# Performance work log

Measured on AMD Instinct MI355X. Metric: run time of the kernel, lower is better.

## Reference

```python
import jax, jax.numpy as jnp
import numpy as np

D = 2048          # hidden_size
N = 16            # num query heads
K = 8             # num kv heads
G = N // K        # GQA groups
H = 128           # head_dim (== head_dim_original, already padded)
T_NOISE = 1024
T_PAD = 1024
MAX_KV = 4096
THETA = 1000000.0
EPS = 1e-6
SM_SCALE = H ** -0.5
NEG = -1e30


def apply_rope(x, pos):
    # x: (T, heads, H); rotate-half (NeoX/Qwen) convention over full head_dim
    half = H // 2
    inv_freq = 1.0 / (THETA ** (jnp.arange(half, dtype=jnp.float32) / half))
    ang = pos.astype(jnp.float32)[:, None] * inv_freq[None, :]      # (T, half)
    cos = jnp.cos(ang)[:, None, :]
    sin = jnp.sin(ang)[:, None, :]
    x1, x2 = x[..., :half], x[..., half:]
    return jnp.concatenate([x1 * cos - x2 * sin, x2 * cos + x1 * sin], axis=-1)


def rms_norm(x, scale):
    var = jnp.mean(jnp.square(x), axis=-1, keepdims=True)
    return x * jax.lax.rsqrt(var + EPS) * scale


def setup_inputs() -> dict:
    key = jax.random.key(0)
    ks = jax.random.split(key, 10)
    cache_len = 1024
    actual_ctx = 768
    u = lambda k, shape: jax.random.uniform(k, shape, jnp.float32) * 0.01  # nnx uniform init
    return {
        "x_noise": jax.random.normal(ks[0], (T_NOISE, D), jnp.float32),
        "target_hidden": jax.random.normal(ks[1], (T_PAD, D), jnp.float32),
        "noise_positions": jnp.arange(T_NOISE, dtype=jnp.int32) + cache_len + actual_ctx,
        "ctx_positions": jnp.arange(T_PAD, dtype=jnp.int32) + cache_len,
        "kv_cache_k": jax.random.normal(ks[2], (1, N, MAX_KV, H), jnp.float32),
        "kv_cache_v": jax.random.normal(ks[3], (1, N, MAX_KV, H), jnp.float32),
        "cache_len": cache_len,
        "actual_ctx_count": actual_ctx,
        "Wq": u(ks[4], (D, N, H)),
        "Wk": u(ks[5], (D, K, H)),
        "Wv": u(ks[6], (D, K, H)),
        "Wo": u(ks[7], (N, H, D)),
        "q_scale": u(ks[8], (H,)),
        "k_scale": u(ks[9], (H,)),
    }


def reference(x_noise, target_hidden, noise_positions, ctx_positions,
              kv_cache_k, kv_cache_v, cache_len, actual_ctx_count,
              Wq, Wk, Wv, Wo, q_scale, k_scale):
    T_noise = x_noise.shape[0]
    T_padded = target_hidden.shape[0]
    # Q projection + RMSNorm + RoPE
    q = jnp.einsum('td,dnh->tnh', x_noise, Wq)
    q = apply_rope(rms_norm(q, q_scale), noise_positions)              # (Tq, N, H)
    # K/V over [context, noise]
    x_new = jnp.concatenate([target_hidden, x_noise], axis=0)
    k_new = jnp.einsum('td,dkh->tkh', x_new, Wk)
    v_new = jnp.einsum('td,dkh->tkh', x_new, Wv)
    new_positions = jnp.concatenate([ctx_positions, noise_positions], axis=0)
    k_new = apply_rope(rms_norm(k_new, k_scale), new_positions)
    # GQA expand before cache write (matches original)
    if G > 1:
        k_new = jnp.repeat(k_new, G, axis=1)
        v_new = jnp.repeat(v_new, G, axis=1)
    # Phase A: masked context write at cache_len
    ctx_mask = (jnp.arange(T_padded) < actual_ctx_count)[:, None, None]
    k_ctx = jnp.where(ctx_mask, k_new[:T_padded], 0.0)
    v_ctx = jnp.where(ctx_mask, v_new[:T_padded], 0.0)
    to4d = lambda a: a.transpose(1, 0, 2)[None]                        # (1, N, T, H)
    kv_cache_k = jax.lax.dynamic_update_slice(kv_cache_k, to4d(k_ctx), (0, 0, cache_len, 0))
    kv_cache_v = jax.lax.dynamic_update_slice(kv_cache_v, to4d(v_ctx), (0, 0, cache_len, 0))
    # Phase B: noise write at cache_len + actual_ctx_count
    noise_start = cache_len + actual_ctx_count
    kv_cache_k = jax.lax.dynamic_update_slice(kv_cache_k, to4d(k_new[T_padded:]), (0, 0, noise_start, 0))
    kv_cache_v = jax.lax.dynamic_update_slice(kv_cache_v, to4d(v_new[T_padded:]), (0, 0, noise_start, 0))
    new_cache_len = noise_start + T_noise
    # Non-causal attention over full cache, padding masked (segment_ids semantics)
    kv_valid = jnp.arange(MAX_KV) < new_cache_len                      # (MAX_KV,)
    scores = jnp.einsum('qnh,nkh->nqk', q, kv_cache_k[0]) * SM_SCALE   # (N, Tq, MAX_KV)
    scores = jnp.where(kv_valid[None, None, :], scores, NEG)
    probs = jax.nn.softmax(scores, axis=-1)
    attn = jnp.einsum('nqk,nkh->qnh', probs, kv_cache_v[0])            # (Tq, N, H)
    output = jnp.einsum('qnh,nhd->qd', attn, Wo)                       # (Tq, D)
    return (output, kv_cache_k, kv_cache_v)
```

## Files before the change

### kernel.cpp

```cpp
#include <hip/hip_runtime.h>
#include <hip/hip_bf16.h>
#include <math.h>

#define D 2048
#define NH 16
#define KHD 8
#define HD 128
#define T_NOISE 1024
#define T_PAD 1024
#define MAX_KV 4096
#define SM_SCALE 0.08838834764831845f

typedef __attribute__((ext_vector_type(8))) short short8;
typedef __attribute__((ext_vector_type(4))) short short4v;
typedef __attribute__((ext_vector_type(4))) float f32x4;

__device__ __forceinline__ unsigned short f2bf(float f) {
    union { float f; unsigned u; } v; v.f = f;
    unsigned r = v.u + 0x7fff + ((v.u >> 16) & 1);
    return (unsigned short)(r >> 16);
}
__device__ __forceinline__ float bf2f(short s) {
    union { unsigned u; float f; } v; v.u = ((unsigned)(unsigned short)s) << 16;
    return v.f;
}
__device__ __forceinline__ void gload16(const void* g, void* l) {
    __builtin_amdgcn_global_load_lds(
        (const __attribute__((address_space(1))) unsigned int*)g,
        (__attribute__((address_space(3))) unsigned int*)l, 16, 0, 0);
}
__device__ __forceinline__ unsigned cvtpk(float lo, float hi) {
    unsigned r;
    asm("v_cvt_pk_bf16_f32 %0, %1, %2" : "=v"(r) : "v"(lo), "v"(hi));
    return r;
}

__global__ __launch_bounds__(256)
void cast_concat(const float* __restrict__ A0, const float* __restrict__ A1,
                 short* __restrict__ out, int splitElems) {
    int i = (blockIdx.x * 256 + threadIdx.x) * 8;
    const float* src = (i < splitElems) ? (A0 + i) : (A1 + (i - splitElems));
    float4 f0 = *(const float4*)src;
    float4 f1 = *(const float4*)(src + 4);
    short8 s;
    s[0] = (short)f2bf(f0.x); s[1] = (short)f2bf(f0.y);
    s[2] = (short)f2bf(f0.z); s[3] = (short)f2bf(f0.w);
    s[4] = (short)f2bf(f1.x); s[5] = (short)f2bf(f1.y);
    s[6] = (short)f2bf(f1.z); s[7] = (short)f2bf(f1.w);
    *(short8*)(out + i) = s;
}

__global__ __launch_bounds__(256)
void conv_transpose(const float* __restrict__ W, short* __restrict__ Wt,
                    int R, int C) {
    __shared__ short t[64][72];
    int tid = threadIdx.x;
    int r0 = blockIdx.y * 64, c0 = blockIdx.x * 64;
    int rl = tid >> 4, cl4 = (tid & 15) * 4;
    #pragma unroll
    for (int j = 0; j < 4; ++j) {
        int r = rl + j * 16;
        float4 f = *(const float4*)(W + (size_t)(r0 + r) * C + c0 + cl4);
        t[cl4 + 0][r] = (short)f2bf(f.x);
        t[cl4 + 1][r] = (short)f2bf(f.y);
        t[cl4 + 2][r] = (short)f2bf(f.z);
        t[cl4 + 3][r] = (short)f2bf(f.w);
    }
    __syncthreads();
    #pragma unroll
    for (int j = 0; j < 2; ++j) {
        int idx = tid + j * 256;
        int cr = idx >> 3, rc8 = (idx & 7) * 8;
        *(short8*)(Wt + (size_t)(c0 + cr) * R + r0 + rc8) = *(const short8*)&t[cr][rc8];
    }
}

__global__ __launch_bounds__(256)
void gemm_qkv(const short* __restrict__ xbf, const short* __restrict__ Btp,
              short* __restrict__ k_tmpb, short* __restrict__ v_tmpb,
              short* __restrict__ q_tmpb) {
    const int n0 = blockIdx.x * 128;
    const int m0 = blockIdx.y * 128;
    const bool isQ = (n0 >= 2048);
    if (isQ && m0 >= 1024) return;
    const short* A = xbf + (isQ ? (size_t)1024 * 2048 : 0);

    __shared__ __align__(16) short As[128 * 32];
    __shared__ __align__(16) short Bs[128 * 32];
    const int tid = threadIdx.x;
    const int w = tid >> 6, lane = tid & 63;
    const int g = lane >> 4, li = lane & 15;
    const int wr = w >> 1, wc = w & 1;

    f32x4 acc[4][4];
    #pragma unroll
    for (int mi = 0; mi < 4; ++mi)
        #pragma unroll
        for (int ni = 0; ni < 4; ++ni) {
            acc[mi][ni][0] = 0.f; acc[mi][ni][1] = 0.f;
            acc[mi][ni][2] = 0.f; acc[mi][ni][3] = 0.f;
        }

    for (int k0 = 0; k0 < 2048; k0 += 32) {
        #pragma unroll
        for (int i = 0; i < 2; ++i) {
            int idx = i * 256 + w * 64 + lane;
            int row = idx >> 2, slot = idx & 3;
            gload16(A + (size_t)(m0 + row) * 2048 + k0 + slot * 8,
                    (char*)As + (size_t)(i * 256 + w * 64) * 16);
            gload16(Btp + (size_t)(n0 + row) * 2048 + k0 + slot * 8,
                    (char*)Bs + (size_t)(i * 256 + w * 64) * 16);
        }
        __syncthreads();
        short8 af[4], bf[4];
        #pragma unroll
        for (int mi = 0; mi < 4; ++mi)
            af[mi] = *(const short8*)&As[(wr * 64 + mi * 16 + li) * 32 + g * 8];
        #pragma unroll
        for (int ni = 0; ni < 4; ++ni)
            bf[ni] = *(const short8*)&Bs[(wc * 64 + ni * 16 + li) * 32 + g * 8];
        #pragma unroll
        for (int mi = 0; mi < 4; ++mi)
            #pragma unroll
            for (int ni = 0; ni < 4; ++ni)
                acc[mi][ni] = __builtin_amdgcn_mfma_f32_16x16x32_bf16(
                    af[mi], bf[ni], acc[mi][ni], 0, 0, 0);
        __syncthreads();
    }
    short* cp; int cbase, ldc2;
    if (n0 < 1024)      { cp = k_tmpb; cbase = 0;    ldc2 = 1024; }
    else if (n0 < 2048) { cp = v_tmpb; cbase = 1024; ldc2 = 1024; }
    else                { cp = q_tmpb; cbase = 2048; ldc2 = 2048; }
    #pragma unroll
    for (int mi = 0; mi < 4; ++mi)
        #pragma unroll
        for (int ni = 0; ni < 4; ++ni) {
            int n = n0 + wc * 64 + ni * 16 + li - cbase;
            #pragma unroll
            for (int r = 0; r < 4; ++r) {
                int m = m0 + wr * 64 + mi * 16 + 4 * g + r;
                cp[(size_t)m * ldc2 + n] = (short)f2bf(acc[mi][ni][r]);
            }
        }
}

__global__ __launch_bounds__(256)
void gemm_bf16(const short* __restrict__ A, const short* __restrict__ Bt,
               float* __restrict__ C0, float* __restrict__ C1,
               int csplit, int ldc, int K, int M) {
    __shared__ __align__(16) short As[128 * 32];
    __shared__ __align__(16) short Bs[128 * 32];
    const int tid = threadIdx.x;
    const int w = tid >> 6, lane = tid & 63;
    const int g = lane >> 4, li = lane & 15;
    const int wr = w >> 1, wc = w & 1;
    const int m0 = blockIdx.y * 128, n0 = blockIdx.x * 128;

    f32x4 acc[4][4];
    #pragma unroll
    for (int mi = 0; mi < 4; ++mi)
        #pragma unroll
        for (int ni = 0; ni < 4; ++ni) {
            acc[mi][ni][0] = 0.f; acc[mi][ni][1] = 0.f;
            acc[mi][ni][2] = 0.f; acc[mi][ni][3] = 0.f;
        }

    for (int k0 = 0; k0 < K; k0 += 32) {
        #pragma unroll
        for (int i = 0; i < 2; ++i) {
            int idx = i * 256 + w * 64 + lane;
            int row = idx >> 2, slot = idx & 3;
            gload16(A + (size_t)(m0 + row) * K + k0 + slot * 8,
                    (char*)As + (size_t)(i * 256 + w * 64) * 16);
            gload16(Bt + (size_t)(n0 + row) * K + k0 + slot * 8,
                    (char*)Bs + (size_t)(i * 256 + w * 64) * 16);
        }
        __syncthreads();
        short8 af[4], bf[4];
        #pragma unroll
        for (int mi = 0; mi < 4; ++mi)
            af[mi] = *(const short8*)&As[(wr * 64 + mi * 16 + li) * 32 + g * 8];
        #pragma unroll
        for (int ni = 0; ni < 4; ++ni)
            bf[ni] = *(const short8*)&Bs[(wc * 64 + ni * 16 + li) * 32 + g * 8];
        #pragma unroll
        for (int mi = 0; mi < 4; ++mi)
            #pragma unroll
            for (int ni = 0; ni < 4; ++ni)
                acc[mi][ni] = __builtin_amdgcn_mfma_f32_16x16x32_bf16(
                    af[mi], bf[ni], acc[mi][ni], 0, 0, 0);
        __syncthreads();
    }
    #pragma unroll
    for (int mi = 0; mi < 4; ++mi) {
        #pragma unroll
        for (int ni = 0; ni < 4; ++ni) {
            int n = n0 + wc * 64 + ni * 16 + li;
            float* cp; int cn;
            if (n < csplit) { cp = C0; cn = n; } else { cp = C1; cn = n - csplit; }
            #pragma unroll
            for (int r = 0; r < 4; ++r) {
                int m = m0 + wr * 64 + mi * 16 + 4 * g + r;
                cp[(size_t)m * ldc + cn] = acc[mi][ni][r];
            }
        }
    }
}

__global__ __launch_bounds__(128)
void rmsrope_bf(short* __restrict__ x, int hpt,
                const int* __restrict__ posA, const int* __restrict__ posB,
                int splitT, const float* __restrict__ scale, float post) {
    __shared__ float red[128];
    __shared__ float nrm[128];
    int row = blockIdx.x;
    int h = threadIdx.x;
    float v = bf2f(x[(size_t)row * HD + h]);
    red[h] = v * v;
    __syncthreads();
    #pragma unroll
    for (int off = 64; off > 0; off >>= 1) {
        if (h < off) red[h] += red[h + off];
        __syncthreads();
    }
    float inv = rsqrtf(red[0] * (1.0f / 128.0f) + 1e-6f);
    nrm[h] = v * inv * scale[h];
    __syncthreads();
    if (h < 64) {
        int t = row / hpt;
        int pos = (t < splitT) ? posA[t] : posB[t - splitT];
        float inv_freq = expf((float)h * (-13.815510557964274f / 64.0f));
        float ang = (float)pos * inv_freq;
        float c = cosf(ang), s = sinf(ang);
        float x1 = nrm[h], x2 = nrm[h + 64];
        x[(size_t)row * HD + h]      = (short)f2bf((x1 * c - x2 * s) * post);
        x[(size_t)row * HD + h + 64] = (short)f2bf((x2 * c + x1 * s) * post);
    }
}

__global__ __launch_bounds__(256)
void cache_scatter2(const float* __restrict__ in_k, const float* __restrict__ in_v,
                    const short* __restrict__ k_tmpb, const short* __restrict__ v_tmpb,
                    float* __restrict__ out_k, float* __restrict__ out_v,
                    short* __restrict__ kbf, short* __restrict__ vbf,
                    const int* __restrict__ clp, const int* __restrict__ acp) {
    const int cache_len = clp[0], actx = acp[0];
    const int noise_start = cache_len + actx;
    const int new_len = noise_start + T_NOISE;
    int i = blockIdx.x * 256 + threadIdx.x;
    int n = i >> 16;
    int rem = i & 65535;
    int pos = rem >> 4;
    int h8 = (rem & 15) << 3;
    size_t co = ((size_t)(n * MAX_KV + pos)) * HD + h8;
    short8 ks8, vs8;
    if (pos >= cache_len && pos < new_len) {
        int tkn = (pos < noise_start) ? (pos - cache_len) : (T_PAD + (pos - noise_start));
        size_t so = ((size_t)(tkn * KHD + (n >> 1))) * HD + h8;
        ks8 = *(const short8*)(k_tmpb + so);
        vs8 = *(const short8*)(v_tmpb + so);
        float4 a, b;
        a.x = bf2f(ks8[0]); a.y = bf2f(ks8[1]); a.z = bf2f(ks8[2]); a.w = bf2f(ks8[3]);
        b.x = bf2f(ks8[4]); b.y = bf2f(ks8[5]); b.z = bf2f(ks8[6]); b.w = bf2f(ks8[7]);
        *(float4*)(out_k + co) = a; *(float4*)(out_k + co + 4) = b;
        a.x = bf2f(vs8[0]); a.y = bf2f(vs8[1]); a.z = bf2f(vs8[2]); a.w = bf2f(vs8[3]);
        b.x = bf2f(vs8[4]); b.y = bf2f(vs8[5]); b.z = bf2f(vs8[6]); b.w = bf2f(vs8[7]);
        *(float4*)(out_v + co) = a; *(float4*)(out_v + co + 4) = b;
    } else {
        float4 ka = *(const float4*)(in_k + co);
        float4 kb = *(const float4*)(in_k + co + 4);
        float4 va = *(const float4*)(in_v + co);
        float4 vb = *(const float4*)(in_v + co + 4);
        *(float4*)(out_k + co) = ka; *(float4*)(out_k + co + 4) = kb;
        *(float4*)(out_v + co) = va; *(float4*)(out_v + co + 4) = vb;
        ks8[0] = (short)f2bf(ka.x); ks8[1] = (short)f2bf(ka.y);
        ks8[2] = (short)f2bf(ka.z); ks8[3] = (short)f2bf(ka.w);
        ks8[4] = (short)f2bf(kb.x); ks8[5] = (short)f2bf(kb.y);
        ks8[6] = (short)f2bf(kb.z); ks8[7] = (short)f2bf(kb.w);
        vs8[0] = (short)f2bf(va.x); vs8[1] = (short)f2bf(va.y);
        vs8[2] = (short)f2bf(va.z); vs8[3] = (short)f2bf(va.w);
        vs8[4] = (short)f2bf(vb.x); vs8[5] = (short)f2bf(vb.y);
        vs8[6] = (short)f2bf(vb.z); vs8[7] = (short)f2bf(vb.w);
    }
    *(short8*)(kbf + co) = ks8;
    *(short8*)(vbf + co) = vs8;
}

#define VBUF(b) ((b) * 8448)

__device__ __forceinline__ short4v tr_read(unsigned addr) {
    short4v d;
    asm volatile("ds_read_b64_tr_b16 %0, %1" : "=v"(d) : "v"(addr));
    return d;
}

__global__ __launch_bounds__(128, 3)
void attn_mfma(const short* __restrict__ qbf, const short* __restrict__ kbf,
               const short* __restrict__ vbf, short* __restrict__ opA,
               short* __restrict__ opB, float* __restrict__ mlpart,
               const int* __restrict__ clp, const int* __restrict__ acp) {
    __shared__ __align__(16) char smem[16896];
    const int tid  = threadIdx.x;
    const int w    = tid >> 6;
    const int lane = tid & 63;
    const int g    = lane >> 4;
    const int li   = lane & 15;
    const int bid  = blockIdx.x;
    const int head = 2 * (bid & 7) + ((bid >> 3) & 1);
    const int rest = bid >> 4;
    const int q0   = (rest & 15) * 64;
    const int kvs  = rest >> 4;
    const int new_len = clp[0] + acp[0] + T_NOISE;
    const int ntiles  = (new_len + 31) >> 5;
    const int ntq     = (ntiles + 3) >> 2;

    const short* kb_g = kbf + (size_t)head * MAX_KV * HD;
    const short* vb_g = vbf + (size_t)head * MAX_KV * HD;

    short8 qf[2][4];
    #pragma unroll
    for (int sub = 0; sub < 2; ++sub) {
        const short* qp = qbf + ((size_t)(q0 + w * 32 + sub * 16 + li) * NH + head) * HD;
        #pragma unroll
        for (int ks = 0; ks < 4; ++ks) qf[sub][ks] = *(const short8*)(qp + 32 * ks + 8 * g);
    }

    f32x4 acc[2][8];
    #pragma unroll
    for (int sub = 0; sub < 2; ++sub)
        #pragma unroll
        for (int n = 0; n < 8; ++n) {
            acc[sub][n][0] = 0.f; acc[sub][n][1] = 0.f;
            acc[sub][n][2] = 0.f; acc[sub][n][3] = 0.f;
        }
    float m[2], l[2];
    m[0] = -INFINITY; m[1] = -INFINITY; l[0] = 0.f; l[1] = 0.f;

    const int vrloc = 4 * (lane >> 3) + ((lane >> 1) & 3);
    const int vcof  = (lane & 1) * 8;

    auto STAGE = [&](int tt, int bb) {
        const int base = (kvs * ntq + tt) * 32;
        #pragma unroll
        for (int i2 = 0; i2 < 4; ++i2) {
            const int ht = w * 4 + i2;
            gload16(vb_g + ((size_t)(base + vrloc) << 7) + ht * 16 + vcof,
                    smem + VBUF(bb) + ht * 1056);
        }
    };

    STAGE(0, 0);
    __syncthreads();

    for (int t = 0; t < ntq; ++t) {
        const int b = t & 1;
        if (t + 1 < ntq) STAGE(t + 1, b ^ 1);
        const int pos0 = (kvs * ntq + t) << 5;
        f32x4 s0[2], s1[2];
        #pragma unroll
        for (int sub = 0; sub < 2; ++sub) {
            s0[sub][0]=0.f; s0[sub][1]=0.f; s0[sub][2]=0.f; s0[sub][3]=0.f;
            s1[sub] = s0[sub];
        }
        {
            const short* kr0 = kb_g + ((size_t)(pos0 + li) << 7) + g * 8;
            const short* kr1 = kr0 + (16 << 7);
            #pragma unroll
            for (int ks = 0; ks < 4; ++ks) {
                short8 k0 = *(const short8*)(kr0 + ks * 32);
                short8 k1 = *(const short8*)(kr1 + ks * 32);
                #pragma unroll
                for (int sub = 0; sub < 2; ++sub) {
                    s0[sub] = __builtin_amdgcn_mfma_f32_16x16x32_bf16(k0, qf[sub][ks], s0[sub], 0, 0, 0);
                    s1[sub] = __builtin_amdgcn_mfma_f32_16x16x32_bf16(k1, qf[sub][ks], s1[sub], 0, 0, 0);
                }
            }
        }
        short8 pa[2];
        #pragma unroll
        for (int sub = 0; sub < 2; ++sub) {
            #pragma unroll
            for (int r = 0; r < 4; ++r) {
                if (pos0 + 4 * g + r >= new_len)      s0[sub][r] = -1e30f;
                if (pos0 + 16 + 4 * g + r >= new_len) s1[sub][r] = -1e30f;
            }
            float tm = fmaxf(fmaxf(fmaxf(s0[sub][0], s0[sub][1]), fmaxf(s0[sub][2], s0[sub][3])),
                             fmaxf(fmaxf(s1[sub][0], s1[sub][1]), fmaxf(s1[sub][2], s1[sub][3])));
            tm = fmaxf(tm, __shfl_xor(tm, 16));
            tm = fmaxf(tm, __shfl_xor(tm, 32));
            const float mn = fmaxf(m[sub], tm);
            const float alpha = __expf(m[sub] - mn);
            float p0[4], p1[4];
            float rs = 0.f;
            #pragma unroll
            for (int r = 0; r < 4; ++r) {
                p0[r] = __expf(s0[sub][r] - mn);
                p1[r] = __expf(s1[sub][r] - mn);
                rs += p0[r] + p1[r];
            }
            rs += __shfl_xor(rs, 16);
            rs += __shfl_xor(rs, 32);
            l[sub] = l[sub] * alpha + rs;
            m[sub] = mn;
            #pragma unroll
            for (int n = 0; n < 8; ++n) {
                acc[sub][n][0] *= alpha; acc[sub][n][1] *= alpha;
                acc[sub][n][2] *= alpha; acc[sub][n][3] *= alpha;
            }
            unsigned w0 = cvtpk(p0[0], p0[1]), w1 = cvtpk(p0[2], p0[3]);
            unsigned w2 = cvtpk(p1[0], p1[1]), w3 = cvtpk(p1[2], p1[3]);
            const bool lowg = (g < 2);
            unsigned a0 = lowg ? w2 : w0, a1 = lowg ? w3 : w1;
            unsigned r0 = __shfl_xor((int)a0, 32), r1 = __shfl_xor((int)a1, 32);
            unsigned o0 = lowg ? w0 : w2, o1 = lowg ? w1 : w3;
            const bool sendOwn = (g == 1 || g == 2);
            unsigned b0 = sendOwn ? o0 : r0, b1 = sendOwn ? o1 : r1;
            unsigned g0_ = __shfl_xor((int)b0, 16), g1_ = __shfl_xor((int)b1, 16);
            union { unsigned u[4]; short8 s; } pau;
            pau.u[0] = (g == 0) ? o0 : (g == 2) ? r0 : g0_;
            pau.u[1] = (g == 0) ? o1 : (g == 2) ? r1 : g1_;
            pau.u[2] = (g == 3) ? o0 : (g == 1) ? r0 : g0_;
            pau.u[3] = (g == 3) ? o1 : (g == 1) ? r1 : g1_;
            pa[sub] = pau.s;
        }
        const unsigned vb0 = (unsigned)(size_t)(smem + VBUF(b)) + g * 256 + li * 8;
        short4v vt[16];
        #pragma unroll
        for (int h2 = 0; h2 < 8; ++h2) {
            vt[2 * h2]     = tr_read(vb0 + h2 * 1056);
            vt[2 * h2 + 1] = tr_read(vb0 + h2 * 1056 + 128);
        }
        asm volatile("s_waitcnt lgkmcnt(0)" ::: "memory");
        __builtin_amdgcn_sched_barrier(0);
        #pragma unroll
        for (int h2 = 0; h2 < 8; ++h2) {
            short8 vf = __builtin_shufflevector(vt[2 * h2], vt[2 * h2 + 1],
                                                0, 1, 2, 3, 4, 5, 6, 7);
            acc[0][h2] = __builtin_amdgcn_mfma_f32_16x16x32_bf16(vf, pa[0], acc[0][h2], 0, 0, 0);
            acc[1][h2] = __builtin_amdgcn_mfma_f32_16x16x32_bf16(vf, pa[1], acc[1][h2], 0, 0, 0);
        }
        __syncthreads();
    }

    short* op = (kvs < 2) ? (opA + (size_t)kvs * 16 * 1024 * 128)
                          : (opB + (size_t)(kvs - 2) * 16 * 1024 * 128);
    #pragma unroll
    for (int sub = 0; sub < 2; ++sub) {
        const int qrow = q0 + w * 32 + sub * 16 + li;
        const size_t ro = ((size_t)(head << 10) + qrow) * 128;
        #pragma unroll
        for (int n = 0; n < 8; ++n) {
            short4v o4;
            o4[0] = (short)f2bf(acc[sub][n][0]); o4[1] = (short)f2bf(acc[sub][n][1]);
            o4[2] = (short)f2bf(acc[sub][n][2]); o4[3] = (short)f2bf(acc[sub][n][3]);
            *(short4v*)(op + ro + 16 * n + 4 * g) = o4;
        }
        if (g == 0) {
            float* ml = mlpart + (((size_t)(kvs * 16 + head) << 10) + qrow) * 2;
            ml[0] = m[sub]; ml[1] = l[sub];
        }
    }
}

__global__ __launch_bounds__(256)
void attn_merge(const short* __restrict__ opA, const short* __restrict__ opB,
                const float* __restrict__ mlpart, short* __restrict__ a_bf) {
    int gid = blockIdx.x * 256 + threadIdx.x;
    int row = gid >> 4;
    int c8  = (gid & 15) * 8;
    int head = row >> 10, q = row & 1023;
    float mg[4], lg[4], mstar = -INFINITY;
    #pragma unroll
    for (int s = 0; s < 4; ++s) {
        const float* ml = mlpart + (((size_t)(s * 16 + head) << 10) + q) * 2;
        mg[s] = ml[0]; lg[s] = ml[1];
        mstar = fmaxf(mstar, mg[s]);
    }
    float cg[4], lstar = 0.f;
    #pragma unroll
    for (int s = 0; s < 4; ++s) { cg[s] = __expf(mg[s] - mstar); lstar += lg[s] * cg[s]; }
    const float inv = 1.0f / lstar;
    float o[8] = {};
    #pragma unroll
    for (int s = 0; s < 4; ++s) {
        const short* op = (s < 2) ? (opA + (size_t)s * 16 * 1024 * 128)
                                  : (opB + (size_t)(s - 2) * 16 * 1024 * 128);
        short8 v = *(const short8*)(op + (((size_t)(head << 10)) + q) * 128 + c8);
        #pragma unroll
        for (int j = 0; j < 8; ++j) o[j] += cg[s] * bf2f(v[j]);
    }
    short8 o8;
    #pragma unroll
    for (int j = 0; j < 8; ++j) o8[j] = (short)f2bf(o[j] * inv);
    *(short8*)(a_bf + (size_t)q * 2048 + head * 128 + c8) = o8;
}

extern "C" void kernel_launch(void* const* d_in, const int* in_sizes, int n_in,
                              void* d_out, int out_size, void* d_ws, size_t ws_size,
                              hipStream_t stream) {
    const float* x_noise       = (const float*)d_in[0];
    const float* target_hidden = (const float*)d_in[1];
    const int*   noise_pos     = (const int*)d_in[2];
    const int*   ctx_pos       = (const int*)d_in[3];
    const float* in_k          = (const float*)d_in[4];
    const float* in_v          = (const float*)d_in[5];
    const int*   clp           = (const int*)d_in[6];
    const int*   acp           = (const int*)d_in[7];
    const float* Wq            = (const float*)d_in[8];
    const float* Wk            = (const float*)d_in[9];
    const float* Wv            = (const float*)d_in[10];
    const float* Wo            = (const float*)d_in[11];
    const float* q_scale       = (const float*)d_in[12];
    const float* k_scale       = (const float*)d_in[13];

    float* out   = (float*)d_out;
    float* out_k = out + (size_t)T_NOISE * D;
    float* out_v = out_k + (size_t)NH * MAX_KV * HD;

    float* ws     = (float*)d_ws;
    const size_t M1 = 1024u * 1024u;
    short* q_tmpb = (short*)ws;
    short* a_bf   = q_tmpb;
    short* k_tmpb = (short*)(ws + 1 * M1);
    short* v_tmpb = (short*)(ws + 2 * M1);
    float* mlpart = (float*)v_tmpb;
    short* xbf    = (short*)(ws + 3 * M1);
    short* opartA = xbf;
    short* btpack = (short*)(ws + 5 * M1);
    short* wo_t   = btpack;
    short* opartB = (short*)(ws + 7 * M1);
    short* kbf    = (short*)(ws + 9 * M1);
    short* vbf    = (short*)(ws + 13 * M1);

    dim3 blk(256);
    cast_concat<<<2048, blk, 0, stream>>>(target_hidden, x_noise, xbf, 1024 * 2048);
    conv_transpose<<<dim3(16, 32), blk, 0, stream>>>(Wk, btpack, 2048, 1024);
    conv_transpose<<<dim3(16, 32), blk, 0, stream>>>(Wv, btpack + (size_t)1024 * 2048, 2048, 1024);
    conv_transpose<<<dim3(32, 32), blk, 0, stream>>>(Wq, btpack + (size_t)2048 * 2048, 2048, 2048);
    gemm_qkv<<<dim3(32, 16), blk, 0, stream>>>(xbf, btpack, k_tmpb, v_tmpb, q_tmpb);
    conv_transpose<<<dim3(32, 32), blk, 0, stream>>>(Wo, wo_t, 2048, 2048);
    rmsrope_bf<<<1024 * 16, 128, 0, stream>>>(q_tmpb, NH, noise_pos, noise_pos, 2048,
                                              q_scale, SM_SCALE);
    rmsrope_bf<<<2048 * 8, 128, 0, stream>>>(k_tmpb, KHD, ctx_pos, noise_pos, 1024,
                                             k_scale, 1.0f);
    cache_scatter2<<<4096, blk, 0, stream>>>(in_k, in_v, k_tmpb, v_tmpb,
                                             out_k, out_v, kbf, vbf, clp, acp);
    attn_mfma<<<1024, 128, 0, stream>>>(q_tmpb, kbf, vbf, opartA, opartB, mlpart, clp, acp);
    attn_merge<<<1024, blk, 0, stream>>>(opartA, opartB, mlpart, a_bf);
    gemm_bf16<<<dim3(16, 8), blk, 0, stream>>>(
        a_bf, wo_t, out, out, 2048, 2048, 2048, 1024);
}
```

Baseline: 245.5 us.

## Widen attention KV tiles to 64 and use 64-row tiles for output GEMM

The attention kernel now processes 64 KV positions per iteration instead of 32, double-buffering twice as much V in shared memory and doing one softmax rescale per 64 keys. This cuts loop and barrier overhead and amortizes the online-softmax bookkeeping, at the cost of more registers and shared memory, so occupancy is lowered to 2 blocks per CU. Separately, the output projection GEMM uses 64x128 tiles, giving 256 blocks instead of 128 so more CUs are busy on the 1024x2048 output.

```diff
diff --git a/kernel.cpp b/kernel.cpp
--- a/kernel.cpp
+++ b/kernel.cpp
@@ -145,20 +145,19 @@
 }
 
 __global__ __launch_bounds__(256)
-void gemm_bf16(const short* __restrict__ A, const short* __restrict__ Bt,
-               float* __restrict__ C0, float* __restrict__ C1,
-               int csplit, int ldc, int K, int M) {
-    __shared__ __align__(16) short As[128 * 32];
+void gemm_bf16_64(const short* __restrict__ A, const short* __restrict__ Bt,
+                  float* __restrict__ C, int ldc, int K) {
+    __shared__ __align__(16) short As[64 * 32];
     __shared__ __align__(16) short Bs[128 * 32];
     const int tid = threadIdx.x;
     const int w = tid >> 6, lane = tid & 63;
     const int g = lane >> 4, li = lane & 15;
     const int wr = w >> 1, wc = w & 1;
-    const int m0 = blockIdx.y * 128, n0 = blockIdx.x * 128;
-
-    f32x4 acc[4][4];
-    #pragma unroll
-    for (int mi = 0; mi < 4; ++mi)
+    const int m0 = blockIdx.y * 64, n0 = blockIdx.x * 128;
+
+    f32x4 acc[2][4];
+    #pragma unroll
+    for (int mi = 0; mi < 2; ++mi)
         #pragma unroll
         for (int ni = 0; ni < 4; ++ni) {
             acc[mi][ni][0] = 0.f; acc[mi][ni][1] = 0.f;
@@ -166,25 +165,29 @@
         }
 
     for (int k0 = 0; k0 < K; k0 += 32) {
+        {
+            int idx = w * 64 + lane;
+            int row = idx >> 2, slot = idx & 3;
+            gload16(A + (size_t)(m0 + row) * K + k0 + slot * 8,
+                    (char*)As + (size_t)(w * 64) * 16);
+        }
         #pragma unroll
         for (int i = 0; i < 2; ++i) {
             int idx = i * 256 + w * 64 + lane;
             int row = idx >> 2, slot = idx & 3;
-            gload16(A + (size_t)(m0 + row) * K + k0 + slot * 8,
-                    (char*)As + (size_t)(i * 256 + w * 64) * 16);
             gload16(Bt + (size_t)(n0 + row) * K + k0 + slot * 8,
                     (char*)Bs + (size_t)(i * 256 + w * 64) * 16);
         }
         __syncthreads();
-        short8 af[4], bf[4];
-        #pragma unroll
-        for (int mi = 0; mi < 4; ++mi)
-            af[mi] = *(const short8*)&As[(wr * 64 + mi * 16 + li) * 32 + g * 8];
+        short8 af[2], bf[4];
+        #pragma unroll
+        for (int mi = 0; mi < 2; ++mi)
+            af[mi] = *(const short8*)&As[(wr * 32 + mi * 16 + li) * 32 + g * 8];
         #pragma unroll
         for (int ni = 0; ni < 4; ++ni)
             bf[ni] = *(const short8*)&Bs[(wc * 64 + ni * 16 + li) * 32 + g * 8];
         #pragma unroll
-        for (int mi = 0; mi < 4; ++mi)
+        for (int mi = 0; mi < 2; ++mi)
             #pragma unroll
             for (int ni = 0; ni < 4; ++ni)
                 acc[mi][ni] = __builtin_amdgcn_mfma_f32_16x16x32_bf16(
@@ -192,19 +195,16 @@
         __syncthreads();
     }
     #pragma unroll
-    for (int mi = 0; mi < 4; ++mi) {
+    for (int mi = 0; mi < 2; ++mi)
         #pragma unroll
         for (int ni = 0; ni < 4; ++ni) {
             int n = n0 + wc * 64 + ni * 16 + li;
-            float* cp; int cn;
-            if (n < csplit) { cp = C0; cn = n; } else { cp = C1; cn = n - csplit; }
             #pragma unroll
             for (int r = 0; r < 4; ++r) {
-                int m = m0 + wr * 64 + mi * 16 + 4 * g + r;
-                cp[(size_t)m * ldc + cn] = acc[mi][ni][r];
-            }
-        }
-    }
+                int m = m0 + wr * 32 + mi * 16 + 4 * g + r;
+                C[(size_t)m * ldc + n] = acc[mi][ni][r];
+            }
+        }
 }
 
 __global__ __launch_bounds__(128)
@@ -286,7 +286,7 @@
     *(short8*)(vbf + co) = vs8;
 }
 
-#define VBUF(b) ((b) * 8448)
+#define VBUF(b) ((b) * 16896)
 
 __device__ __forceinline__ short4v tr_read(unsigned addr) {
     short4v d;
@@ -294,12 +294,12 @@
     return d;
 }
 
-__global__ __launch_bounds__(128, 3)
+__global__ __launch_bounds__(128, 2)
 void attn_mfma(const short* __restrict__ qbf, const short* __restrict__ kbf,
                const short* __restrict__ vbf, short* __restrict__ opA,
                short* __restrict__ opB, float* __restrict__ mlpart,
                const int* __restrict__ clp, const int* __restrict__ acp) {
-    __shared__ __align__(16) char smem[16896];
+    __shared__ __align__(16) char smem[33792];
     const int tid  = threadIdx.x;
     const int w    = tid >> 6;
     const int lane = tid & 63;
@@ -311,7 +311,7 @@
     const int q0   = (rest & 15) * 64;
     const int kvs  = rest >> 4;
     const int new_len = clp[0] + acp[0] + T_NOISE;
-    const int ntiles  = (new_len + 31) >> 5;
+    const int ntiles  = (new_len + 63) >> 6;
     const int ntq     = (ntiles + 3) >> 2;
 
     const short* kb_g = kbf + (size_t)head * MAX_KV * HD;
@@ -340,13 +340,33 @@
     const int vcof  = (lane & 1) * 8;
 
     auto STAGE = [&](int tt, int bb) {
-        const int base = (kvs * ntq + tt) * 32;
-        #pragma unroll
-        for (int i2 = 0; i2 < 4; ++i2) {
-            const int ht = w * 4 + i2;
-            gload16(vb_g + ((size_t)(base + vrloc) << 7) + ht * 16 + vcof,
-                    smem + VBUF(bb) + ht * 1056);
-        }
+        const int base = (kvs * ntq + tt) * 64;
+        #pragma unroll
+        for (int half = 0; half < 2; ++half)
+            #pragma unroll
+            for (int i2 = 0; i2 < 4; ++i2) {
+                const int ht = w * 4 + i2;
+                gload16(vb_g + ((size_t)(base + half * 32 + vrloc) << 7) + ht * 16 + vcof,
+                        smem + VBUF(bb) + half * 8448 + ht * 1056);
+            }
+    };
+
+    auto mkfrag = [&](const float* pA, const float* pB) -> short8 {
+        unsigned w0 = cvtpk(pA[0], pA[1]), w1 = cvtpk(pA[2], pA[3]);
+        unsigned w2 = cvtpk(pB[0], pB[1]), w3 = cvtpk(pB[2], pB[3]);
+        const bool lowg = (g < 2);
+        unsigned a0 = lowg ? w2 : w0, a1 = lowg ? w3 : w1;
+        unsigned r0 = __shfl_xor((int)a0, 32), r1 = __shfl_xor((int)a1, 32);
+        unsigned o0 = lowg ? w0 : w2, o1 = lowg ? w1 : w3;
+        const bool sendOwn = (g == 1 || g == 2);
+        unsigned b0 = sendOwn ? o0 : r0, b1 = sendOwn ? o1 : r1;
+        unsigned g0_ = __shfl_xor((int)b0, 16), g1_ = __shfl_xor((int)b1, 16);
+        union { unsigned u[4]; short8 s; } pau;
+        pau.u[0] = (g == 0) ? o0 : (g == 2) ? r0 : g0_;
+        pau.u[1] = (g == 0) ? o1 : (g == 2) ? r1 : g1_;
+        pau.u[2] = (g == 3) ? o0 : (g == 1) ? r0 : g0_;
+        pau.u[3] = (g == 3) ? o1 : (g == 1) ? r1 : g1_;
+        return pau.s;
     };
 
     STAGE(0, 0);
@@ -355,49 +375,55 @@
     for (int t = 0; t < ntq; ++t) {
         const int b = t & 1;
         if (t + 1 < ntq) STAGE(t + 1, b ^ 1);
-        const int pos0 = (kvs * ntq + t) << 5;
-        f32x4 s0[2], s1[2];
+        const int pos0 = (kvs * ntq + t) << 6;
+        f32x4 s[4][2];
+        #pragma unroll
+        for (int j = 0; j < 4; ++j)
+            #pragma unroll
+            for (int sub = 0; sub < 2; ++sub) {
+                s[j][sub][0] = 0.f; s[j][sub][1] = 0.f;
+                s[j][sub][2] = 0.f; s[j][sub][3] = 0.f;
+            }
+        {
+            const short* kr = kb_g + ((size_t)(pos0 + li) << 7) + g * 8;
+            #pragma unroll
+            for (int ks = 0; ks < 4; ++ks) {
+                #pragma unroll
+                for (int j = 0; j < 4; ++j) {
+                    short8 kf = *(const short8*)(kr + (size_t)j * 16 * HD + ks * 32);
+                    s[j][0] = __builtin_amdgcn_mfma_f32_16x16x32_bf16(kf, qf[0][ks], s[j][0], 0, 0, 0);
+                    s[j][1] = __builtin_amdgcn_mfma_f32_16x16x32_bf16(kf, qf[1][ks], s[j][1], 0, 0, 0);
+                }
+            }
+        }
+        #pragma unroll
+        for (int j = 0; j < 4; ++j)
+            #pragma unroll
+            for (int r = 0; r < 4; ++r)
+                if (pos0 + 16 * j + 4 * g + r >= new_len) {
+                    s[j][0][r] = -1e30f; s[j][1][r] = -1e30f;
+                }
+        short8 pa[2][2];
         #pragma unroll
         for (int sub = 0; sub < 2; ++sub) {
-            s0[sub][0]=0.f; s0[sub][1]=0.f; s0[sub][2]=0.f; s0[sub][3]=0.f;
-            s1[sub] = s0[sub];
-        }
-        {
-            const short* kr0 = kb_g + ((size_t)(pos0 + li) << 7) + g * 8;
-            const short* kr1 = kr0 + (16 << 7);
-            #pragma unroll
-            for (int ks = 0; ks < 4; ++ks) {
-                short8 k0 = *(const short8*)(kr0 + ks * 32);
-                short8 k1 = *(const short8*)(kr1 + ks * 32);
+            float tm = -INFINITY;
+            #pragma unroll
+            for (int j = 0; j < 4; ++j)
                 #pragma unroll
-                for (int sub = 0; sub < 2; ++sub) {
-                    s0[sub] = __builtin_amdgcn_mfma_f32_16x16x32_bf16(k0, qf[sub][ks], s0[sub], 0, 0, 0);
-                    s1[sub] = __builtin_amdgcn_mfma_f32_16x16x32_bf16(k1, qf[sub][ks], s1[sub], 0, 0, 0);
-                }
-            }
-        }
-        short8 pa[2];
-        #pragma unroll
-        for (int sub = 0; sub < 2; ++sub) {
-            #pragma unroll
-            for (int r = 0; r < 4; ++r) {
-                if (pos0 + 4 * g + r >= new_len)      s0[sub][r] = -1e30f;
-                if (pos0 + 16 + 4 * g + r >= new_len) s1[sub][r] = -1e30f;
-            }
-            float tm = fmaxf(fmaxf(fmaxf(s0[sub][0], s0[sub][1]), fmaxf(s0[sub][2], s0[sub][3])),
-                             fmaxf(fmaxf(s1[sub][0], s1[sub][1]), fmaxf(s1[sub][2], s1[sub][3])));
+                for (int r = 0; r < 4; ++r) tm = fmaxf(tm, s[j][sub][r]);
             tm = fmaxf(tm, __shfl_xor(tm, 16));
             tm = fmaxf(tm, __shfl_xor(tm, 32));
             const float mn = fmaxf(m[sub], tm);
             const float alpha = __expf(m[sub] - mn);
-            float p0[4], p1[4];
+            float p[4][4];
             float rs = 0.f;
             #pragma unroll
-            for (int r = 0; r < 4; ++r) {
-                p0[r] = __expf(s0[sub][r] - mn);
-                p1[r] = __expf(s1[sub][r] - mn);
-                rs += p0[r] + p1[r];
-            }
+            for (int j = 0; j < 4; ++j)
+                #pragma unroll
+                for (int r = 0; r < 4; ++r) {
+                    p[j][r] = __expf(s[j][sub][r] - mn);
+                    rs += p[j][r];
+                }
             rs += __shfl_xor(rs, 16);
             rs += __shfl_xor(rs, 32);
             l[sub] = l[sub] * alpha + rs;
@@ -407,37 +433,28 @@
                 acc[sub][n][0] *= alpha; acc[sub][n][1] *= alpha;
                 acc[sub][n][2] *= alpha; acc[sub][n][3] *= alpha;
             }
-            unsigned w0 = cvtpk(p0[0], p0[1]), w1 = cvtpk(p0[2], p0[3]);
-            unsigned w2 = cvtpk(p1[0], p1[1]), w3 = cvtpk(p1[2], p1[3]);
-            const bool lowg = (g < 2);
-            unsigned a0 = lowg ? w2 : w0, a1 = lowg ? w3 : w1;
-            unsigned r0 = __shfl_xor((int)a0, 32), r1 = __shfl_xor((int)a1, 32);
-            unsigned o0 = lowg ? w0 : w2, o1 = lowg ? w1 : w3;
-            const bool sendOwn = (g == 1 || g == 2);
-            unsigned b0 = sendOwn ? o0 : r0, b1 = sendOwn ? o1 : r1;
-            unsigned g0_ = __shfl_xor((int)b0, 16), g1_ = __shfl_xor((int)b1, 16);
-            union { unsigned u[4]; short8 s; } pau;
-            pau.u[0] = (g == 0) ? o0 : (g == 2) ? r0 : g0_;
-            pau.u[1] = (g == 0) ? o1 : (g == 2) ? r1 : g1_;
-            pau.u[2] = (g == 3) ? o0 : (g == 1) ? r0 : g0_;
-            pau.u[3] = (g == 3) ? o1 : (g == 1) ? r1 : g1_;
-            pa[sub] = pau.s;
-        }
-        const unsigned vb0 = (unsigned)(size_t)(smem + VBUF(b)) + g * 256 + li * 8;
-        short4v vt[16];
-        #pragma unroll
-        for (int h2 = 0; h2 < 8; ++h2) {
-            vt[2 * h2]     = tr_read(vb0 + h2 * 1056);
-            vt[2 * h2 + 1] = tr_read(vb0 + h2 * 1056 + 128);
-        }
-        asm volatile("s_waitcnt lgkmcnt(0)" ::: "memory");
-        __builtin_amdgcn_sched_barrier(0);
-        #pragma unroll
-        for (int h2 = 0; h2 < 8; ++h2) {
-            short8 vf = __builtin_shufflevector(vt[2 * h2], vt[2 * h2 + 1],
-                                                0, 1, 2, 3, 4, 5, 6, 7);
-            acc[0][h2] = __builtin_amdgcn_mfma_f32_16x16x32_bf16(vf, pa[0], acc[0][h2], 0, 0, 0);
-            acc[1][h2] = __builtin_amdgcn_mfma_f32_16x16x32_bf16(vf, pa[1], acc[1][h2], 0, 0, 0);
+            pa[sub][0] = mkfrag(p[0], p[1]);
+            pa[sub][1] = mkfrag(p[2], p[3]);
+        }
+        #pragma unroll
+        for (int half = 0; half < 2; ++half) {
+            const unsigned vb0 = (unsigned)(size_t)(smem + VBUF(b)) + half * 8448
+                               + g * 256 + li * 8;
+            short4v vt[16];
+            #pragma unroll
+            for (int h2 = 0; h2 < 8; ++h2) {
+                vt[2 * h2]     = tr_read(vb0 + h2 * 1056);
+                vt[2 * h2 + 1] = tr_read(vb0 + h2 * 1056 + 128);
+            }
+            asm volatile("s_waitcnt lgkmcnt(0)" ::: "memory");
+            __builtin_amdgcn_sched_barrier(0);
+            #pragma unroll
+            for (int h2 = 0; h2 < 8; ++h2) {
+                short8 vf = __builtin_shufflevector(vt[2 * h2], vt[2 * h2 + 1],
+                                                    0, 1, 2, 3, 4, 5, 6, 7);
+                acc[0][h2] = __builtin_amdgcn_mfma_f32_16x16x32_bf16(vf, pa[0][half], acc[0][h2], 0, 0, 0);
+                acc[1][h2] = __builtin_amdgcn_mfma_f32_16x16x32_bf16(vf, pa[1][half], acc[1][h2], 0, 0, 0);
+            }
         }
         __syncthreads();
     }
@@ -547,6 +564,5 @@
                                              out_k, out_v, kbf, vbf, clp, acp);
     attn_mfma<<<1024, 128, 0, stream>>>(q_tmpb, kbf, vbf, opartA, opartB, mlpart, clp, acp);
     attn_merge<<<1024, blk, 0, stream>>>(opartA, opartB, mlpart, a_bf);
-    gemm_bf16<<<dim3(16, 8), blk, 0, stream>>>(
-        a_bf, wo_t, out, out, 2048, 2048, 2048, 1024);
-}
+    gemm_bf16_64<<<dim3(16, 16), blk, 0, stream>>>(a_bf, wo_t, out, 2048, 2048);
+}
```

New measurement: 230.8 us. 6.0% less time.
